# Kernel optimization log

Hardware: AMD Instinct MI355X
Metric: run time of the kernel (lower is better)

Reference implementation:

```python
import jax, jax.numpy as jnp
import numpy as np

N_NODES = 100000
N_EDGES = 3200000
NODE_F = 256
EDGE_F = 16
N_HEAD = 8
OUT_F = 256
NEG_SLOPE = 0.2
BN_EPS = 1e-5


def _seg_softmax(e, idx, num_segments):
    # numerically stable segment softmax over edges grouped by idx
    m = jax.ops.segment_max(e, idx, num_segments=num_segments)
    ex = jnp.exp(e - m[idx])
    s = jax.ops.segment_sum(ex, idx, num_segments=num_segments)
    return ex / s[idx]


def setup_inputs() -> dict:
    key = jax.random.key(0)
    ks = jax.random.split(key, 16)
    inp = {}
    inp["feat_src"] = jax.random.normal(ks[0], (N_NODES, NODE_F), jnp.float32)
    inp["feat_edge"] = jax.random.normal(ks[1], (N_EDGES, EDGE_F), jnp.float32)
    inp["src"] = jax.random.randint(ks[2], (N_EDGES,), 0, N_NODES, jnp.int32)
    inp["dst"] = jax.random.randint(ks[3], (N_EDGES,), 0, N_NODES, jnp.int32)
    def xav(k, fan_in, fan_out):
        # xavier_normal with relu gain sqrt(2)
        std = np.sqrt(2.0) * np.sqrt(2.0 / (fan_in + fan_out))
        return jax.random.normal(k, (fan_in, fan_out), jnp.float32) * std
    inp["W_prop_src"] = xav(ks[4], NODE_F, N_HEAD)
    inp["W_attn_src"] = xav(ks[5], NODE_F, N_HEAD)
    inp["W_attn_dst"] = xav(ks[6], NODE_F, N_HEAD)
    inp["W_attn_edge"] = xav(ks[7], EDGE_F, N_HEAD)
    inp["bn_gamma"] = jnp.ones((N_HEAD,), jnp.float32)
    inp["bn_beta"] = jnp.zeros((N_HEAD,), jnp.float32)
    inp["W_agg"] = xav(ks[8], N_HEAD, OUT_F)
    inp["b_agg"] = jnp.zeros((OUT_F,), jnp.float32)
    inp["W_apply_dst"] = xav(ks[9], NODE_F, OUT_F)
    inp["b_apply_dst"] = jnp.zeros((OUT_F,), jnp.float32)
    inp["W_apply"] = xav(ks[10], OUT_F, OUT_F)
    inp["b_apply"] = jnp.zeros((OUT_F,), jnp.float32)
    return inp


def reference(feat_src, feat_edge, src, dst, W_prop_src, W_attn_src, W_attn_dst,
              W_attn_edge, bn_gamma, bn_beta, W_agg, b_agg, W_apply_dst,
              b_apply_dst, W_apply, b_apply):
    leaky = lambda x: jnp.where(x >= 0, x, NEG_SLOPE * x)
    feat_dst = feat_src  # non-block graph
    feat_src_fc = feat_src @ W_prop_src            # [N, H]
    attn_src = feat_src @ W_attn_src               # [N, H]
    attn_dst = feat_dst @ W_attn_dst               # [N, H]
    attn_edge = feat_edge @ W_attn_edge            # [E, H]
    e = attn_src[src] + attn_dst[dst] + attn_edge  # [E, H]
    e = leaky(e)                                   # edge_att_actv = leaky_relu
    # dual softmax: geometric mean of dst- and src-normalized softmaxes
    a_dst = jnp.clip(_seg_softmax(e, dst, N_NODES), 1e-9)
    a_src = jnp.clip(_seg_softmax(e, src, N_NODES), 1e-9)
    a = jnp.sqrt(a_dst * a_src)                    # [E, H]
    msg_sum = jax.ops.segment_sum(feat_src_fc[src] * a, dst, num_segments=N_NODES)  # [N, H]
    # BatchNorm1d (training mode: batch statistics over nodes, biased var)
    mu = jnp.mean(msg_sum, axis=0)
    var = jnp.mean((msg_sum - mu) ** 2, axis=0)
    h = (msg_sum - mu) / jnp.sqrt(var + BN_EPS) * bn_gamma + bn_beta
    rst = h @ W_agg + b_agg                        # [N, OUT]
    rst = rst + feat_dst @ W_apply_dst + b_apply_dst
    rst = leaky(rst)
    rst = rst @ W_apply + b_apply
    return rst
```

## Files before the change

kernel.cpp:

```cpp
#include <hip/hip_runtime.h>

#define LRELU(x) ((x) >= 0.0f ? (x) : 0.2f * (x))

typedef __attribute__((ext_vector_type(8))) short short8;
typedef __attribute__((ext_vector_type(4))) float f32x4;

__device__ __forceinline__ unsigned short f2bf(float f) {
    union { float f; unsigned int u; } v; v.f = f;
    unsigned int u = v.u;
    u += 0x7FFFu + ((u >> 16) & 1u);
    return (unsigned short)(u >> 16);
}

__device__ __forceinline__ float bf2f(unsigned short u) {
    union { unsigned int u; float f; } v; v.u = ((unsigned int)u) << 16;
    return v.f;
}

__device__ __forceinline__ void atomic_pk_add_bf16(unsigned short* p, unsigned int pk) {
    asm volatile("global_atomic_pk_add_bf16 %0, %1, off"
                 :: "v"(p), "v"(pk) : "memory");
}

__global__ __launch_bounds__(256) void k_node_tables(
    const float* __restrict__ feat,
    const float* __restrict__ Wp, const float* __restrict__ Was,
    const float* __restrict__ Wad,
    float* __restrict__ fc, float* __restrict__ as_t, float* __restrict__ ad_t,
    int N)
{
    __shared__ float Wl[3 * 2048];
    for (int i = threadIdx.x; i < 3 * 2048; i += 256) {
        float v;
        if (i < 2048)      v = Wp[i];
        else if (i < 4096) v = Was[i - 2048];
        else               v = Wad[i - 4096];
        Wl[i] = v;
    }
    __syncthreads();
    int gid = blockIdx.x * 256 + threadIdx.x;
    int n = gid >> 3, h = gid & 7;
    if (n >= N) return;
    const float4* f4 = (const float4*)(feat + (size_t)n * 256);
    float aP = 0.f, aS = 0.f, aD = 0.f;
#pragma unroll 8
    for (int k4 = 0; k4 < 64; ++k4) {
        float4 f = f4[k4];
        int b = k4 * 32 + h;
        aP += f.x * Wl[b]        + f.y * Wl[b + 8]        + f.z * Wl[b + 16]        + f.w * Wl[b + 24];
        aS += f.x * Wl[2048 + b] + f.y * Wl[2048 + b + 8] + f.z * Wl[2048 + b + 16] + f.w * Wl[2048 + b + 24];
        aD += f.x * Wl[4096 + b] + f.y * Wl[4096 + b + 8] + f.z * Wl[4096 + b + 16] + f.w * Wl[4096 + b + 24];
    }
    fc[gid] = aP; as_t[gid] = aS; ad_t[gid] = aD;
}

__device__ __forceinline__ float edge_ex(
    const float* __restrict__ feat_edge, const float* Wl,
    const float* __restrict__ as_t, const float* __restrict__ ad_t,
    int e, int h, int s, int d)
{
    const float4* fe = (const float4*)(feat_edge + (size_t)e * 16);
    float4 f0 = fe[0], f1 = fe[1], f2 = fe[2], f3 = fe[3];
    float ae = f0.x * Wl[h]      + f0.y * Wl[h + 8]   + f0.z * Wl[h + 16]  + f0.w * Wl[h + 24]
             + f1.x * Wl[h + 32] + f1.y * Wl[h + 40]  + f1.z * Wl[h + 48]  + f1.w * Wl[h + 56]
             + f2.x * Wl[h + 64] + f2.y * Wl[h + 72]  + f2.z * Wl[h + 80]  + f2.w * Wl[h + 88]
             + f3.x * Wl[h + 96] + f3.y * Wl[h + 104] + f3.z * Wl[h + 112] + f3.w * Wl[h + 120];
    float ev = as_t[s * 8 + h] + ad_t[d * 8 + h] + ae;
    ev = LRELU(ev);
    return __expf(ev);
}

__global__ __launch_bounds__(256) void k_edge1(
    const float* __restrict__ feat_edge,
    const int* __restrict__ src, const int* __restrict__ dst,
    const float* __restrict__ We,
    const float* __restrict__ as_t, const float* __restrict__ ad_t,
    unsigned short* __restrict__ sum_dst_bf,
    unsigned short* __restrict__ sum_src_bf,
    unsigned short* __restrict__ exd, int E)
{
    __shared__ float Wl[128];
    if (threadIdx.x < 128) Wl[threadIdx.x] = We[threadIdx.x];
    __syncthreads();
    int gid = blockIdx.x * 256 + threadIdx.x;
    int e = gid >> 3, h = gid & 7;
    if (e >= E) return;
    int s = src[e], d = dst[e];
    float ex = edge_ex(feat_edge, Wl, as_t, ad_t, e, h, s, d);
    unsigned short exb = f2bf(ex);
    exd[gid] = exb;
    float exn = __shfl_xor(ex, 1);
    if ((h & 1) == 0) {
        unsigned int pk = (unsigned int)exb | ((unsigned int)f2bf(exn) << 16);
        atomic_pk_add_bf16(sum_dst_bf + d * 8 + h, pk);
        atomic_pk_add_bf16(sum_src_bf + s * 8 + h, pk);
    }
}

__global__ __launch_bounds__(256) void k_edge2(
    const unsigned short* __restrict__ exd,
    const int* __restrict__ src, const int* __restrict__ dst,
    const unsigned short* __restrict__ sum_dst_bf,
    const unsigned short* __restrict__ sum_src_bf,
    const float* __restrict__ fc, float* __restrict__ msg, int E)
{
    int gid = blockIdx.x * 256 + threadIdx.x;
    int e = gid >> 3, h = gid & 7;
    if (e >= E) return;
    int s = src[e], d = dst[e];
    float ex = bf2f(exd[gid]);
    float Sd = bf2f(sum_dst_bf[d * 8 + h]);
    float Ss = bf2f(sum_src_bf[s * 8 + h]);
    float a_d = fmaxf(ex / Sd, 1e-9f);
    float a_s = fmaxf(ex / Ss, 1e-9f);
    atomicAdd(&msg[d * 8 + h], fc[s * 8 + h] * sqrtf(a_d * a_s));
}

__global__ __launch_bounds__(256) void k_bn_stats(
    const float* __restrict__ msg, float* __restrict__ accum, int N)
{
    __shared__ float s1[8], s2[8];
    if (threadIdx.x < 8) { s1[threadIdx.x] = 0.f; s2[threadIdx.x] = 0.f; }
    __syncthreads();
    int h = threadIdx.x & 7;
    float a1 = 0.f, a2 = 0.f;
    int total = N * 8;
    for (int i = blockIdx.x * 256 + threadIdx.x; i < total; i += gridDim.x * 256) {
        float x = msg[i];
        a1 += x; a2 += x * x;
    }
    atomicAdd(&s1[h], a1);
    atomicAdd(&s2[h], a2);
    __syncthreads();
    if (threadIdx.x < 8) {
        atomicAdd(&accum[threadIdx.x], s1[threadIdx.x]);
        atomicAdd(&accum[8 + threadIdx.x], s2[threadIdx.x]);
    }
}

__global__ __launch_bounds__(256) void k_prep(
    const float* __restrict__ W1, const float* __restrict__ Wagg,
    const float* __restrict__ W2,
    const float* __restrict__ b_agg, const float* __restrict__ b1,
    const float* __restrict__ b2,
    unsigned short* __restrict__ B1t, unsigned short* __restrict__ B2t,
    float* __restrict__ bias1, float* __restrict__ bias2)
{
    int idx = blockIdx.x * 256 + threadIdx.x;
    if (idx < 73728) {
        int c = idx >> 13, rem = idx & 8191;
        int n = rem >> 5, k = rem & 31;
        float v;
        if (c < 8) v = W1[(c * 32 + k) * 256 + n];
        else       v = (k < 8) ? Wagg[k * 256 + n] : 0.f;
        B1t[idx] = f2bf(v);
    } else if (idx < 139264) {
        int j = idx - 73728;
        int c = j >> 13, rem = j & 8191;
        int n = rem >> 5, k = rem & 31;
        B2t[j] = f2bf(W2[(c * 32 + k) * 256 + n]);
    } else if (idx < 139520) {
        int n = idx - 139264;
        bias1[n] = b_agg[n] + b1[n];
    } else if (idx < 139776) {
        int n = idx - 139520;
        bias2[n] = b2[n];
    }
}

#define ASTRIDE 296

__global__ __launch_bounds__(256, 2) void k_fused_apply(
    const float* __restrict__ feat, const float* __restrict__ msg,
    const float* __restrict__ accum,
    const float* __restrict__ gamma, const float* __restrict__ beta,
    const unsigned short* __restrict__ B1t,
    const unsigned short* __restrict__ B2t,
    const float* __restrict__ bias1, const float* __restrict__ bias2,
    float* __restrict__ out, int N)
{
    __shared__ __align__(16) unsigned short As[64 * ASTRIDE];
    __shared__ __align__(16) unsigned short Bs[8192];

    int tid = threadIdx.x;
    int row0 = blockIdx.x * 64;

#pragma unroll
    for (int t = 0; t < 16; ++t) {
        int i = tid + t * 256;
        int r = i >> 6, k4 = i & 63;
        float4 f = make_float4(0.f, 0.f, 0.f, 0.f);
        if (row0 + r < N)
            f = ((const float4*)(feat + (size_t)(row0 + r) * 256))[k4];
        ushort4 b;
        b.x = f2bf(f.x); b.y = f2bf(f.y); b.z = f2bf(f.z); b.w = f2bf(f.w);
        *(ushort4*)&As[r * ASTRIDE + k4 * 4] = b;
    }
#pragma unroll
    for (int t = 0; t < 8; ++t) {
        int e = tid + t * 256;
        int r = e >> 5, c = e & 31;
        float v = 0.f;
        if (c < 8 && row0 + r < N) {
            float invN = 1.0f / (float)N;
            float mu = accum[c] * invN;
            float var = accum[8 + c] * invN - mu * mu;
            float rstd = rsqrtf(var + 1e-5f);
            v = (msg[(size_t)(row0 + r) * 8 + c] - mu) * rstd * gamma[c] + beta[c];
        }
        As[r * ASTRIDE + 256 + c] = f2bf(v);
    }

    int wave = tid >> 6;
    int lane = tid & 63;
    int n16  = lane & 15;
    int quad = lane >> 4;
    int col0 = wave * 64;

    f32x4 acc[4][4];
#pragma unroll
    for (int rt = 0; rt < 4; ++rt)
#pragma unroll
        for (int ct = 0; ct < 4; ++ct)
            acc[rt][ct] = (f32x4){0.f, 0.f, 0.f, 0.f};

    for (int kc = 0; kc < 9; ++kc) {
        __syncthreads();
#pragma unroll
        for (int t = 0; t < 4; ++t) {
            int i = tid + t * 256;
            ((float4*)Bs)[i] = ((const float4*)(B1t + kc * 8192))[i];
        }
        __syncthreads();
        int kbase = kc * 32;
        short8 af[4], bf[4];
#pragma unroll
        for (int rt = 0; rt < 4; ++rt)
            af[rt] = *(const short8*)&As[(rt * 16 + n16) * ASTRIDE + kbase + quad * 8];
#pragma unroll
        for (int ct = 0; ct < 4; ++ct)
            bf[ct] = *(const short8*)&Bs[(col0 + ct * 16 + n16) * 32 + quad * 8];
#pragma unroll
        for (int rt = 0; rt < 4; ++rt)
#pragma unroll
            for (int ct = 0; ct < 4; ++ct)
                acc[rt][ct] = __builtin_amdgcn_mfma_f32_16x16x32_bf16(
                    af[rt], bf[ct], acc[rt][ct], 0, 0, 0);
    }

    float bi[4];
#pragma unroll
    for (int ct = 0; ct < 4; ++ct) bi[ct] = bias1[col0 + ct * 16 + n16];
    __syncthreads();
#pragma unroll
    for (int rt = 0; rt < 4; ++rt)
#pragma unroll
        for (int ct = 0; ct < 4; ++ct)
#pragma unroll
            for (int r = 0; r < 4; ++r) {
                float v = acc[rt][ct][r] + bi[ct];
                v = LRELU(v);
                int row = rt * 16 + quad * 4 + r;
                int col = col0 + ct * 16 + n16;
                As[row * ASTRIDE + col] = f2bf(v);
            }

#pragma unroll
    for (int rt = 0; rt < 4; ++rt)
#pragma unroll
        for (int ct = 0; ct < 4; ++ct)
            acc[rt][ct] = (f32x4){0.f, 0.f, 0.f, 0.f};

    for (int kc = 0; kc < 8; ++kc) {
        __syncthreads();
#pragma unroll
        for (int t = 0; t < 4; ++t) {
            int i = tid + t * 256;
            ((float4*)Bs)[i] = ((const float4*)(B2t + kc * 8192))[i];
        }
        __syncthreads();
        int kbase = kc * 32;
        short8 af[4], bf[4];
#pragma unroll
        for (int rt = 0; rt < 4; ++rt)
            af[rt] = *(const short8*)&As[(rt * 16 + n16) * ASTRIDE + kbase + quad * 8];
#pragma unroll
        for (int ct = 0; ct < 4; ++ct)
            bf[ct] = *(const short8*)&Bs[(col0 + ct * 16 + n16) * 32 + quad * 8];
#pragma unroll
        for (int rt = 0; rt < 4; ++rt)
#pragma unroll
            for (int ct = 0; ct < 4; ++ct)
                acc[rt][ct] = __builtin_amdgcn_mfma_f32_16x16x32_bf16(
                    af[rt], bf[ct], acc[rt][ct], 0, 0, 0);
    }

    float bi2[4];
#pragma unroll
    for (int ct = 0; ct < 4; ++ct) bi2[ct] = bias2[col0 + ct * 16 + n16];
#pragma unroll
    for (int rt = 0; rt < 4; ++rt)
#pragma unroll
        for (int r = 0; r < 4; ++r) {
            int row = row0 + rt * 16 + quad * 4 + r;
            if (row < N) {
#pragma unroll
                for (int ct = 0; ct < 4; ++ct) {
                    int col = col0 + ct * 16 + n16;
                    out[(size_t)row * 256 + col] = acc[rt][ct][r] + bi2[ct];
                }
            }
        }
}

extern "C" void kernel_launch(void* const* d_in, const int* in_sizes, int n_in,
                              void* d_out, int out_size, void* d_ws, size_t ws_size,
                              hipStream_t stream)
{
    const float* feat      = (const float*)d_in[0];
    const float* feat_edge = (const float*)d_in[1];
    const int*   src       = (const int*)d_in[2];
    const int*   dst       = (const int*)d_in[3];
    const float* W_prop    = (const float*)d_in[4];
    const float* W_as      = (const float*)d_in[5];
    const float* W_ad      = (const float*)d_in[6];
    const float* W_edge    = (const float*)d_in[7];
    const float* bn_gamma  = (const float*)d_in[8];
    const float* bn_beta   = (const float*)d_in[9];
    const float* W_agg     = (const float*)d_in[10];
    const float* b_agg     = (const float*)d_in[11];
    const float* W1        = (const float*)d_in[12];
    const float* b1        = (const float*)d_in[13];
    const float* W2        = (const float*)d_in[14];
    const float* b2        = (const float*)d_in[15];
    float* out = (float*)d_out;

    int N = in_sizes[0] / 256;
    int E = in_sizes[2];
    int N8 = N * 8;

    char* base = (char*)d_ws;
    size_t o = 0;
    auto take = [&](size_t bytes) -> char* {
        char* p = base + o;
        o = (o + bytes + 63) & ~(size_t)63;
        return p;
    };
    unsigned short* sum_dst_bf = (unsigned short*)take((size_t)N8 * 2);
    unsigned short* sum_src_bf = (unsigned short*)take((size_t)N8 * 2);
    float* msg   = (float*)take((size_t)N8 * sizeof(float));
    float* accum = (float*)take(16 * sizeof(float));
    size_t zero_bytes = o;
    float* fc    = (float*)take((size_t)N8 * sizeof(float));
    float* as_t  = (float*)take((size_t)N8 * sizeof(float));
    float* ad_t  = (float*)take((size_t)N8 * sizeof(float));
    float* bias1 = (float*)take(256 * sizeof(float));
    float* bias2 = (float*)take(256 * sizeof(float));
    unsigned short* B1t = (unsigned short*)take(73728 * sizeof(unsigned short));
    unsigned short* B2t = (unsigned short*)take(65536 * sizeof(unsigned short));
    unsigned short* exd = (unsigned short*)take((size_t)E * 8 * sizeof(unsigned short));
    (void)ws_size;

    hipMemsetAsync(d_ws, 0, zero_bytes, stream);

    int gridN8 = (N8 + 255) / 256;
    int gridE8 = (E * 8 + 255) / 256;
    int gridF  = (N + 63) / 64;

    k_prep<<<546, 256, 0, stream>>>(W1, W_agg, W2, b_agg, b1, b2,
                                    B1t, B2t, bias1, bias2);
    k_node_tables<<<gridN8, 256, 0, stream>>>(feat, W_prop, W_as, W_ad,
                                              fc, as_t, ad_t, N);
    k_edge1<<<gridE8, 256, 0, stream>>>(feat_edge, src, dst, W_edge,
                                        as_t, ad_t, sum_dst_bf, sum_src_bf,
                                        exd, E);
    k_edge2<<<gridE8, 256, 0, stream>>>(exd, src, dst, sum_dst_bf, sum_src_bf,
                                        fc, msg, E);
    k_bn_stats<<<512, 256, 0, stream>>>(msg, accum, N);
    k_fused_apply<<<gridF, 256, 0, stream>>>(feat, msg, accum, bn_gamma, bn_beta,
                                             B1t, B2t, bias1, bias2, out, N);
}
```

Measured before the change: 974.0 us.

## Replicate scatter accumulators per XCC with workgroup-scope atomics, then reduce

Edge-softmax denominators and the message scatter now accumulate into eight per-XCC fp32 replicas using workgroup-scope atomics. Because each XCD only touches its own replica, the atomics can resolve in its local L2 instead of going device-wide. Separate reduce kernels then sum the replicas, and the message reduction is fused with the BatchNorm statistics pass. This replaces the packed bf16 atomics with fp32 ones, which raises precision, but it multiplies the zeroed memset region and the reduction traffic by eight. If the workspace is too small, the code skips storing per-edge exp values and recomputes them in the second edge kernel.

```diff
diff --git a/kernel.cpp b/kernel.cpp
--- a/kernel.cpp
+++ b/kernel.cpp
@@ -17,9 +17,14 @@
     return v.f;
 }
 
-__device__ __forceinline__ void atomic_pk_add_bf16(unsigned short* p, unsigned int pk) {
-    asm volatile("global_atomic_pk_add_bf16 %0, %1, off"
-                 :: "v"(p), "v"(pk) : "memory");
+__device__ __forceinline__ int xcc_id() {
+    unsigned x;
+    asm("s_getreg_b32 %0, hwreg(HW_REG_XCC_ID)" : "=s"(x));
+    return (int)(x & 7);
+}
+
+__device__ __forceinline__ void l2_atomic_add(float* p, float v) {
+    __hip_atomic_fetch_add(p, v, __ATOMIC_RELAXED, __HIP_MEMORY_SCOPE_WORKGROUP);
 }
 
 __global__ __launch_bounds__(256) void k_node_tables(
@@ -65,7 +70,7 @@
              + f1.x * Wl[h + 32] + f1.y * Wl[h + 40]  + f1.z * Wl[h + 48]  + f1.w * Wl[h + 56]
              + f2.x * Wl[h + 64] + f2.y * Wl[h + 72]  + f2.z * Wl[h + 80]  + f2.w * Wl[h + 88]
              + f3.x * Wl[h + 96] + f3.y * Wl[h + 104] + f3.z * Wl[h + 112] + f3.w * Wl[h + 120];
-    float ev = as_t[s * 8 + h] + ad_t[d * 8 + h] + ae;
+    float ev = as_t[(size_t)s * 8 + h] + ad_t[(size_t)d * 8 + h] + ae;
     ev = LRELU(ev);
     return __expf(ev);
 }
@@ -75,9 +80,8 @@
     const int* __restrict__ src, const int* __restrict__ dst,
     const float* __restrict__ We,
     const float* __restrict__ as_t, const float* __restrict__ ad_t,
-    unsigned short* __restrict__ sum_dst_bf,
-    unsigned short* __restrict__ sum_src_bf,
-    unsigned short* __restrict__ exd, int E)
+    float* __restrict__ sdr, unsigned short* __restrict__ exd,
+    int E, int N8)
 {
     __shared__ float Wl[128];
     if (threadIdx.x < 128) Wl[threadIdx.x] = We[threadIdx.x];
@@ -87,47 +91,64 @@
     if (e >= E) return;
     int s = src[e], d = dst[e];
     float ex = edge_ex(feat_edge, Wl, as_t, ad_t, e, h, s, d);
-    unsigned short exb = f2bf(ex);
-    exd[gid] = exb;
-    float exn = __shfl_xor(ex, 1);
-    if ((h & 1) == 0) {
-        unsigned int pk = (unsigned int)exb | ((unsigned int)f2bf(exn) << 16);
-        atomic_pk_add_bf16(sum_dst_bf + d * 8 + h, pk);
-        atomic_pk_add_bf16(sum_src_bf + s * 8 + h, pk);
-    }
+    if (exd) exd[gid] = f2bf(ex);
+    float* rep = sdr + (size_t)xcc_id() * 2 * (size_t)N8;
+    l2_atomic_add(rep + (size_t)d * 8 + h, ex);
+    l2_atomic_add(rep + (size_t)N8 + (size_t)s * 8 + h, ex);
+}
+
+__global__ __launch_bounds__(256) void k_reduce_sums(
+    const float* __restrict__ sdr, float* __restrict__ sums, int total)
+{
+    int i = blockIdx.x * 256 + threadIdx.x;
+    if (i >= total) return;
+    float a = 0.f;
+#pragma unroll
+    for (int x = 0; x < 8; ++x) a += sdr[(size_t)x * total + i];
+    sums[i] = a;
 }
 
 __global__ __launch_bounds__(256) void k_edge2(
     const unsigned short* __restrict__ exd,
+    const float* __restrict__ feat_edge, const float* __restrict__ We,
     const int* __restrict__ src, const int* __restrict__ dst,
-    const unsigned short* __restrict__ sum_dst_bf,
-    const unsigned short* __restrict__ sum_src_bf,
-    const float* __restrict__ fc, float* __restrict__ msg, int E)
-{
+    const float* __restrict__ sums,
+    const float* __restrict__ as_t, const float* __restrict__ ad_t,
+    const float* __restrict__ fc, float* __restrict__ msgr,
+    int E, int N8)
+{
+    __shared__ float Wl[128];
+    if (threadIdx.x < 128) Wl[threadIdx.x] = We[threadIdx.x];
+    __syncthreads();
     int gid = blockIdx.x * 256 + threadIdx.x;
     int e = gid >> 3, h = gid & 7;
     if (e >= E) return;
     int s = src[e], d = dst[e];
-    float ex = bf2f(exd[gid]);
-    float Sd = bf2f(sum_dst_bf[d * 8 + h]);
-    float Ss = bf2f(sum_src_bf[s * 8 + h]);
+    float ex = exd ? bf2f(exd[gid])
+                   : edge_ex(feat_edge, Wl, as_t, ad_t, e, h, s, d);
+    float Sd = sums[(size_t)d * 8 + h];
+    float Ss = sums[(size_t)N8 + (size_t)s * 8 + h];
     float a_d = fmaxf(ex / Sd, 1e-9f);
     float a_s = fmaxf(ex / Ss, 1e-9f);
-    atomicAdd(&msg[d * 8 + h], fc[s * 8 + h] * sqrtf(a_d * a_s));
-}
-
-__global__ __launch_bounds__(256) void k_bn_stats(
-    const float* __restrict__ msg, float* __restrict__ accum, int N)
+    float m = fc[(size_t)s * 8 + h] * sqrtf(a_d * a_s);
+    l2_atomic_add(msgr + (size_t)xcc_id() * (size_t)N8 + (size_t)d * 8 + h, m);
+}
+
+__global__ __launch_bounds__(256) void k_reduce_msg_bn(
+    const float* __restrict__ msgr, float* __restrict__ msg,
+    float* __restrict__ accum, int N8)
 {
     __shared__ float s1[8], s2[8];
     if (threadIdx.x < 8) { s1[threadIdx.x] = 0.f; s2[threadIdx.x] = 0.f; }
     __syncthreads();
     int h = threadIdx.x & 7;
     float a1 = 0.f, a2 = 0.f;
-    int total = N * 8;
-    for (int i = blockIdx.x * 256 + threadIdx.x; i < total; i += gridDim.x * 256) {
-        float x = msg[i];
-        a1 += x; a2 += x * x;
+    for (int i = blockIdx.x * 256 + threadIdx.x; i < N8; i += gridDim.x * 256) {
+        float v = 0.f;
+#pragma unroll
+        for (int x = 0; x < 8; ++x) v += msgr[(size_t)x * N8 + i];
+        msg[i] = v;
+        a1 += v; a2 += v * v;
     }
     atomicAdd(&s1[h], a1);
     atomicAdd(&s2[h], a2);
@@ -346,11 +367,12 @@
         o = (o + bytes + 63) & ~(size_t)63;
         return p;
     };
-    unsigned short* sum_dst_bf = (unsigned short*)take((size_t)N8 * 2);
-    unsigned short* sum_src_bf = (unsigned short*)take((size_t)N8 * 2);
-    float* msg   = (float*)take((size_t)N8 * sizeof(float));
+    float* sdr   = (float*)take((size_t)8 * 2 * N8 * sizeof(float));
+    float* msgr  = (float*)take((size_t)8 * N8 * sizeof(float));
     float* accum = (float*)take(16 * sizeof(float));
     size_t zero_bytes = o;
+    float* sums  = (float*)take((size_t)2 * N8 * sizeof(float));
+    float* msg   = (float*)take((size_t)N8 * sizeof(float));
     float* fc    = (float*)take((size_t)N8 * sizeof(float));
     float* as_t  = (float*)take((size_t)N8 * sizeof(float));
     float* ad_t  = (float*)take((size_t)N8 * sizeof(float));
@@ -358,13 +380,18 @@
     float* bias2 = (float*)take(256 * sizeof(float));
     unsigned short* B1t = (unsigned short*)take(73728 * sizeof(unsigned short));
     unsigned short* B2t = (unsigned short*)take(65536 * sizeof(unsigned short));
+    size_t need_noexd = o;
     unsigned short* exd = (unsigned short*)take((size_t)E * 8 * sizeof(unsigned short));
-    (void)ws_size;
+    size_t need_full = o;
+
+    if (ws_size < need_full) exd = nullptr;
+    (void)need_noexd;
 
     hipMemsetAsync(d_ws, 0, zero_bytes, stream);
 
     int gridN8 = (N8 + 255) / 256;
     int gridE8 = (E * 8 + 255) / 256;
+    int gridS  = (2 * N8 + 255) / 256;
     int gridF  = (N + 63) / 64;
 
     k_prep<<<546, 256, 0, stream>>>(W1, W_agg, W2, b_agg, b1, b2,
@@ -372,11 +399,11 @@
     k_node_tables<<<gridN8, 256, 0, stream>>>(feat, W_prop, W_as, W_ad,
                                               fc, as_t, ad_t, N);
     k_edge1<<<gridE8, 256, 0, stream>>>(feat_edge, src, dst, W_edge,
-                                        as_t, ad_t, sum_dst_bf, sum_src_bf,
-                                        exd, E);
-    k_edge2<<<gridE8, 256, 0, stream>>>(exd, src, dst, sum_dst_bf, sum_src_bf,
-                                        fc, msg, E);
-    k_bn_stats<<<512, 256, 0, stream>>>(msg, accum, N);
+                                        as_t, ad_t, sdr, exd, E, N8);
+    k_reduce_sums<<<gridS, 256, 0, stream>>>(sdr, sums, 2 * N8);
+    k_edge2<<<gridE8, 256, 0, stream>>>(exd, feat_edge, W_edge, src, dst,
+                                        sums, as_t, ad_t, fc, msgr, E, N8);
+    k_reduce_msg_bn<<<512, 256, 0, stream>>>(msgr, msg, accum, N8);
     k_fused_apply<<<gridF, 256, 0, stream>>>(feat, msg, accum, bn_gamma, bn_beta,
                                              B1t, B2t, bias1, bias2, out, N);
 }
```

Measured after the change: 1.027 ms. +5.4%, slower.
